# Kernel optimization log

Hardware: AMD Instinct MI355X
Metric: run time of the kernel (lower is better)

Reference implementation:

```python
import jax, jax.numpy as jnp
import numpy as np

ALPHA = 0.2  # LeakyReLU negative slope
NEG_INF = jnp.float32(-9e15)


def gat_layer(h, mask, W, a, concat):
    """Dense GAT layer (pyGAT style). h: [B,N,Fin], mask: [N,N] bool, W: [Fin,Fout], a: [2*Fout,1]."""
    Wh = h @ W                                   # [B,N,Fout]
    F_out = W.shape[-1]
    e_src = Wh @ a[:F_out]                       # [B,N,1]
    e_dst = Wh @ a[F_out:]                       # [B,N,1]
    e = jax.nn.leaky_relu(e_src + jnp.swapaxes(e_dst, -1, -2), ALPHA)  # [B,N,N]
    att = jnp.where(mask, e, NEG_INF)
    att = jax.nn.softmax(att, axis=-1)
    out = att @ Wh                               # [B,N,Fout]
    return jax.nn.elu(out) if concat else out


def setup_inputs() -> dict:
    key = jax.random.key(0)
    ks = jax.random.split(key, 8)
    B, N, nfeat, nhid, nheads, emb, nclass = 4, 2048, 128, 64, 8, 64, 16
    slices = jax.random.normal(ks[0], (B, N, nfeat), jnp.float32)
    adj = jax.random.randint(ks[1], (N, N), 0, 2, jnp.int32)
    s = 1.0 / float(np.sqrt(nfeat))
    Ws = jax.random.uniform(ks[2], (nheads, nfeat, nhid), jnp.float32, -s, s)
    As = jax.random.uniform(ks[3], (nheads, 2 * nhid, 1), jnp.float32, -s, s)
    W1 = jax.random.uniform(ks[4], (nhid * nheads, emb), jnp.float32, -s, s)
    a1 = jax.random.uniform(ks[5], (2 * emb, 1), jnp.float32, -s, s)
    W2 = jax.random.uniform(ks[6], (emb, nclass), jnp.float32, -s, s)
    a2 = jax.random.uniform(ks[7], (2 * nclass, 1), jnp.float32, -s, s)
    return {"slices": slices, "adj": adj, "Ws": Ws, "As": As,
            "W1": W1, "a1": a1, "W2": W2, "a2": a2}


def reference(slices, adj, Ws, As, W1, a1, W2, a2):
    # Eval mode: dropout = 0 (identity).
    mask = adj > 0                               # [N,N], broadcasts over batch
    # Multi-head GAT with concat=True (ELU inside each head), vectorized over heads.
    heads = jax.vmap(lambda W, a: gat_layer(slices, mask, W, a, True))(Ws, As)  # [H,B,N,nhid]
    H, B, N, nh = heads.shape
    x = jnp.moveaxis(heads, 0, 2).reshape(B, N, H * nh)  # concat along features, head-major
    image_feature = jax.nn.elu(gat_layer(x, mask, W1, a1, False))              # [B,N,emb]
    pre = jax.nn.elu(gat_layer(image_feature, mask, W2, a2, False))            # [B,N,nclass]
    pre = pre[:, 0, :]                                                         # [B,nclass]
    return image_feature, pre
```

## Files before the change

### kernel.cpp

```cpp
#include <hip/hip_runtime.h>
#include <hip/hip_bf16.h>
#include <cstdint>


#define NN 2048

typedef float f32x4 __attribute__((ext_vector_type(4)));
typedef __bf16 bf16x8 __attribute__((ext_vector_type(8)));
typedef _Float16 f16;
typedef _Float16 f16x8 __attribute__((ext_vector_type(8)));

__global__ __launch_bounds__(256) void prep_k(
    const int* __restrict__ adj, unsigned char* __restrict__ pm,
    const float* __restrict__ Ws, __bf16* __restrict__ WsFh, __bf16* __restrict__ WsFl,
    const float* __restrict__ W1, __bf16* __restrict__ W1Fh, __bf16* __restrict__ W1Fl,
    unsigned int* __restrict__ ticket) {
  const int bx = blockIdx.x, t = threadIdx.x;
  if (bx == 0 && t == 0) *ticket = 0u;
  if (bx < 2048) {
    const int i = bx;
#pragma unroll
    for (int jt = 0; jt < 8; ++jt) {
      const int j = jt * 256 + t;
      pm[((long)(j >> 5) << 16) + i * 32 + (j & 31)] =
          adj[(long)i * NN + j] > 0 ? 0xFFu : 0u;
    }
  } else if (bx < 2304) {
    const int idx = (bx - 2048) * 256 + t;
    const int inst = idx >> 13;
    const int rem = idx & 8191;
    const int k = rem >> 6, n = rem & 63;
    const float v = Ws[(long)inst * 8192 + rem];
    const __bf16 vh = (__bf16)v;
    const int pos = ((k >> 5) * 4 + (n >> 4)) * 512 + (((k >> 3) & 3) * 16 + (n & 15)) * 8 + (k & 7);
    WsFh[(long)inst * 8192 + pos] = vh;
    WsFl[(long)inst * 8192 + pos] = (__bf16)(v - (float)vh);
  } else {
    const int idx = (bx - 2304) * 256 + t;
    const int k = idx >> 6, n = idx & 63;
    const float v = W1[idx];
    const __bf16 vh = (__bf16)v;
    const int pos = ((k >> 5) * 4 + (n >> 4)) * 512 + (((k >> 3) & 3) * 16 + (n & 15)) * 8 + (k & 7);
    W1Fh[pos] = vh;
    W1Fl[pos] = (__bf16)(v - (float)vh);
  }
}

struct GemmLd {
  float4 a0, a1;
  bf16x8 bh[4], bl[4];
};

__global__ __launch_bounds__(128) void gemm_mfma_k(
    const float* __restrict__ Aall, const __bf16* __restrict__ WFhi,
    const __bf16* __restrict__ WFlo, const float* __restrict__ avecAll,
    f16* __restrict__ WhBAll, float* __restrict__ Eo, float* __restrict__ Go,
    f16* __restrict__ Fo, f16* __restrict__ Ho,
    int K, long aStrideB) {
  const int bid = blockIdx.x;
  const int xcd = bid & 7, r = bid >> 3;
  const int xblk = r & 63, hh = r >> 6;
  const int head = ((xcd >> 2) << 2) + hh;
  const int p = (head << 2) | (xcd & 3);
  const float* A = Aall + (long)(p & 3) * aStrideB;
  const long wfOff = (long)(p >> 2) * K * 64;
  const bf16x8* BhF = (const bf16x8*)(WFhi + wfOff);
  const bf16x8* BlF = (const bf16x8*)(WFlo + wfOff);

  const int t = threadIdx.x, lane = t & 63, wave = t >> 6;
  const int quad = lane >> 4, lm = lane & 15;
  const int i0w = xblk * 32 + wave * 16;
  const float* Arow = A + (long)(i0w + lm) * K;
  const int kBeg = 0, kEnd = K;

  f32x4 acc[4];
#pragma unroll
  for (int nt = 0; nt < 4; ++nt) acc[nt] = (f32x4){0.f, 0.f, 0.f, 0.f};

  auto LOAD = [&](GemmLd& L, int k0) {
    L.a0 = *(const float4*)(Arow + k0 + quad * 8);
    L.a1 = *(const float4*)(Arow + k0 + quad * 8 + 4);
    const int bbase = (k0 >> 5) * 256 + lane;
#pragma unroll
    for (int nt = 0; nt < 4; ++nt) {
      L.bh[nt] = BhF[bbase + nt * 64];
      L.bl[nt] = BlF[bbase + nt * 64];
    }
  };
  auto STEP = [&](const GemmLd& L) {
    const float av8[8] = {L.a0.x, L.a0.y, L.a0.z, L.a0.w, L.a1.x, L.a1.y, L.a1.z, L.a1.w};
    bf16x8 ah, al;
#pragma unroll
    for (int j = 0; j < 8; ++j) {
      const __bf16 h = (__bf16)av8[j];
      ah[j] = h;
      al[j] = (__bf16)(av8[j] - (float)h);
    }
#pragma unroll
    for (int nt = 0; nt < 4; ++nt) {
      acc[nt] = __builtin_amdgcn_mfma_f32_16x16x32_bf16(ah, L.bh[nt], acc[nt], 0, 0, 0);
      acc[nt] = __builtin_amdgcn_mfma_f32_16x16x32_bf16(al, L.bh[nt], acc[nt], 0, 0, 0);
      acc[nt] = __builtin_amdgcn_mfma_f32_16x16x32_bf16(ah, L.bl[nt], acc[nt], 0, 0, 0);
    }
  };

  GemmLd La, Lb;
  LOAD(La, kBeg);
  for (int k0 = kBeg; k0 < kEnd; k0 += 64) {
    LOAD(Lb, k0 + 32);
    STEP(La);
    LOAD(La, (k0 + 64 < kEnd) ? k0 + 64 : kBeg);
    STEP(Lb);
  }

  const float* av = avecAll + (long)(p >> 2) * 128;
  f16* WhB = WhBAll + (long)p * NN * 64;
  float* E = Eo + (long)p * NN;
  float* G = Go + (long)p * NN;
  f16* F = Fo + (long)p * NN;
  f16* Hh = Ho + (long)p * NN;

  float alo[4], ahi[4];
#pragma unroll
  for (int nt = 0; nt < 4; ++nt) {
    alo[nt] = av[nt * 16 + lm];
    ahi[nt] = av[64 + nt * 16 + lm];
  }
#pragma unroll
  for (int reg = 0; reg < 4; ++reg) {
    float es = 0.f, ed = 0.f;
#pragma unroll
    for (int nt = 0; nt < 4; ++nt) {
      es += acc[nt][reg] * alo[nt];
      ed += acc[nt][reg] * ahi[nt];
    }
#pragma unroll
    for (int m = 1; m < 16; m <<= 1) {
      es += __shfl_xor(es, m);
      ed += __shfl_xor(ed, m);
    }
    if (lm == 0) {
      const int r2 = i0w + quad * 4 + reg;
      E[r2] = __expf(es);
      G[r2] = __expf(0.2f * es);
      F[r2] = (f16)__expf(ed);
      Hh[r2] = (f16)__expf(0.2f * ed);
    }
  }

  const int r0 = i0w + quad * 4;
  const long base = ((long)(r0 >> 5) * 4) * 512 + (((r0 >> 3) & 3) * 16 + lm) * 8 + (r0 & 7);
#pragma unroll
  for (int nt = 0; nt < 4; ++nt) {
    union { f16 h[4]; uint2 u; } pk;
#pragma unroll
    for (int q = 0; q < 4; ++q) pk.h[q] = (f16)acc[nt][q];
    *(uint2*)(WhB + base + nt * 512) = pk.u;
  }
}

__global__ __launch_bounds__(512) void gemm2_k(
    const float* __restrict__ Aall, const __bf16* __restrict__ WFhi,
    const __bf16* __restrict__ WFlo, const float* __restrict__ avec,
    f16* __restrict__ WhBAll, float* __restrict__ Eo, float* __restrict__ Go,
    f16* __restrict__ Fo, f16* __restrict__ Ho) {
  const int p = blockIdx.y;
  const float* A = Aall + (long)p * NN * 512;
  const bf16x8* BhF = (const bf16x8*)WFhi;
  const bf16x8* BlF = (const bf16x8*)WFlo;
  const int t = threadIdx.x, lane = t & 63, wave = t >> 6;
  const int ks = wave & 3, rh = wave >> 2;
  const int quad = lane >> 4, lm = lane & 15;
  const int i0 = blockIdx.x * 32;
  const float* Arow = A + (long)(i0 + rh * 16 + lm) * 512;
  const int kBeg = ks * 128, kEnd = kBeg + 128;

  f32x4 acc[4];
#pragma unroll
  for (int nt = 0; nt < 4; ++nt) acc[nt] = (f32x4){0.f, 0.f, 0.f, 0.f};

  auto LOAD = [&](GemmLd& L, int k0) {
    L.a0 = *(const float4*)(Arow + k0 + quad * 8);
    L.a1 = *(const float4*)(Arow + k0 + quad * 8 + 4);
    const int bbase = (k0 >> 5) * 256 + lane;
#pragma unroll
    for (int nt = 0; nt < 4; ++nt) {
      L.bh[nt] = BhF[bbase + nt * 64];
      L.bl[nt] = BlF[bbase + nt * 64];
    }
  };
  auto STEP = [&](const GemmLd& L) {
    const float av8[8] = {L.a0.x, L.a0.y, L.a0.z, L.a0.w, L.a1.x, L.a1.y, L.a1.z, L.a1.w};
    bf16x8 ah, al;
#pragma unroll
    for (int j = 0; j < 8; ++j) {
      const __bf16 h = (__bf16)av8[j];
      ah[j] = h;
      al[j] = (__bf16)(av8[j] - (float)h);
    }
#pragma unroll
    for (int nt = 0; nt < 4; ++nt) {
      acc[nt] = __builtin_amdgcn_mfma_f32_16x16x32_bf16(ah, L.bh[nt], acc[nt], 0, 0, 0);
      acc[nt] = __builtin_amdgcn_mfma_f32_16x16x32_bf16(al, L.bh[nt], acc[nt], 0, 0, 0);
      acc[nt] = __builtin_amdgcn_mfma_f32_16x16x32_bf16(ah, L.bl[nt], acc[nt], 0, 0, 0);
    }
  };

  GemmLd La, Lb;
  LOAD(La, kBeg);
  for (int k0 = kBeg; k0 < kEnd; k0 += 64) {
    LOAD(Lb, k0 + 32);
    STEP(La);
    LOAD(La, (k0 + 64 < kEnd) ? k0 + 64 : kBeg);
    STEP(Lb);
  }

  __shared__ __align__(16) float red[8][4][64][4];
#pragma unroll
  for (int nt = 0; nt < 4; ++nt) *(f32x4*)&red[wave][nt][lane][0] = acc[nt];
  __syncthreads();

  const int n = lane, rgrp = wave;
  const int rh2 = rgrp >> 2, q2 = rgrp & 3;
  const int ln = q2 * 16 + (n & 15), ntq = n >> 4;
  f32x4 c4 = *(const f32x4*)&red[rh2 * 4 + 0][ntq][ln][0];
#pragma unroll
  for (int ksum = 1; ksum < 4; ++ksum)
    c4 += *(const f32x4*)&red[rh2 * 4 + ksum][ntq][ln][0];

  f32x4 es4 = c4 * avec[n];
  f32x4 ed4 = c4 * avec[64 + n];
#pragma unroll
  for (int m = 1; m < 64; m <<= 1) {
#pragma unroll
    for (int q = 0; q < 4; ++q) {
      es4[q] += __shfl_xor(es4[q], m);
      ed4[q] += __shfl_xor(ed4[q], m);
    }
  }
  const int row0 = i0 + rgrp * 4;
  if (n == 0) {
#pragma unroll
    for (int reg = 0; reg < 4; ++reg) {
      const int row = row0 + reg;
      Eo[(long)p * NN + row] = __expf(es4[reg]);
      Go[(long)p * NN + row] = __expf(0.2f * es4[reg]);
      Fo[(long)p * NN + row] = (f16)__expf(ed4[reg]);
      Ho[(long)p * NN + row] = (f16)__expf(0.2f * ed4[reg]);
    }
  }
  f16* WhB = WhBAll + (long)p * NN * 64;
  union { f16 h[4]; uint2 u; } pk;
#pragma unroll
  for (int reg = 0; reg < 4; ++reg) pk.h[reg] = (f16)c4[reg];
  const long pos = ((long)(row0 >> 5) * 4 + ntq) * 512 +
                   ((((row0 >> 3) & 3) * 16 + (n & 15)) * 8) + (row0 & 7);
  *(uint2*)(WhB + pos) = pk.u;
}

struct KbLd {
  f16x8 F8, H8;
  f16x8 b[4];
  uint2 m[4];
};

__global__ __launch_bounds__(512, 2) void attn_k(
    const f16* __restrict__ WhBAll, const float* __restrict__ Eb,
    const float* __restrict__ Gb, const f16* __restrict__ Fb,
    const f16* __restrict__ Hb, const unsigned char* __restrict__ pm,
    float* __restrict__ out1, int rowStride, long strideB,
    int jsCount, float* __restrict__ partAcc, float* __restrict__ partSum) {
  const int bid = blockIdx.x;
  int p, js, rowblk;
  if (jsCount == 1) {
    const int xcd = bid & 7, r = bid >> 3;
    p = xcd * 4 + (r & 3);
    rowblk = r >> 2;
    js = 0;
  } else {
    const int xcd = bid & 7;
    const int idx = ((xcd & 1) << 4) + (bid >> 3);
    p = xcd >> 1;
    js = idx >> 3;
    rowblk = idx & 7;
  }
  const f16* WhB = WhBAll + (long)p * NN * 64;
  const float* E = Eb + (long)p * NN;
  const float* G = Gb + (long)p * NN;
  const f16* Fg = Fb + (long)p * NN;
  const f16* Hg = Hb + (long)p * NN;
  const int t = threadIdx.x, lane = t & 63, wave = t >> 6;
  const int rw = wave & 3, half = wave >> 2;
  const int quad = lane >> 4, lm = lane & 15;
  const int i0 = rowblk * 256;
  const int rbase = rw * 64;
  const int span = 64 / jsCount;
  const int nIter = span / 2;
  const int kbBeg = js * span + half * nIter, kbEnd = kbBeg + nIter;

  __shared__ __align__(16) float cmb[20480];

  f16x8 ev[4], gv[4];
#pragma unroll
  for (int g = 0; g < 4; ++g) {
    const int r = i0 + rbase + g * 16 + lm;
    const f16 e = (f16)E[r], gg = (f16)G[r];
#pragma unroll
    for (int j = 0; j < 8; ++j) { ev[g][j] = e; gv[g][j] = gg; }
  }

  f16x8 ones;
#pragma unroll
  for (int j = 0; j < 8; ++j) ones[j] = (lm == 0) ? (f16)1.0f : (f16)0.0f;

  f32x4 acc[4][4], sum[4];
#pragma unroll
  for (int g = 0; g < 4; ++g) {
    sum[g] = (f32x4){0.f, 0.f, 0.f, 0.f};
#pragma unroll
    for (int nt = 0; nt < 4; ++nt) acc[g][nt] = (f32x4){0.f, 0.f, 0.f, 0.f};
  }

  const unsigned char* mp[4];
#pragma unroll
  for (int g = 0; g < 4; ++g)
    mp[g] = pm + (long)(i0 + rbase + g * 16 + lm) * 32 + quad * 8;

  auto LD = [&](KbLd& L, int kb) {
    L.F8 = *(const f16x8*)(Fg + kb * 32 + quad * 8);
    L.H8 = *(const f16x8*)(Hg + kb * 32 + quad * 8);
#pragma unroll
    for (int nt = 0; nt < 4; ++nt)
      L.b[nt] = *(const f16x8*)(WhB + (long)kb * 2048 + (nt * 64 + lane) * 8);
#pragma unroll
    for (int g = 0; g < 4; ++g)
      L.m[g] = *(const uint2*)(mp[g] + ((long)kb << 16));
  };
  auto CP = [&](const KbLd& L) {
    union { f16x8 v; uint4 u4; } A[4];
#pragma unroll
    for (int g = 0; g < 4; ++g) {
      A[g].v = __builtin_elementwise_max(ev[g] * L.F8, gv[g] * L.H8);
      A[g].u4.x &= __builtin_amdgcn_perm(0u, L.m[g].x, 0x01010000u);
      A[g].u4.y &= __builtin_amdgcn_perm(0u, L.m[g].x, 0x03030202u);
      A[g].u4.z &= __builtin_amdgcn_perm(0u, L.m[g].y, 0x01010000u);
      A[g].u4.w &= __builtin_amdgcn_perm(0u, L.m[g].y, 0x03030202u);
    }
    __builtin_amdgcn_s_setprio(1);
#pragma unroll
    for (int nt = 0; nt < 4; ++nt) {
#pragma unroll
      for (int g = 0; g < 4; ++g)
        acc[g][nt] = __builtin_amdgcn_mfma_f32_16x16x32_f16(A[g].v, L.b[nt], acc[g][nt], 0, 0, 0);
    }
#pragma unroll
    for (int g = 0; g < 4; ++g)
      sum[g] = __builtin_amdgcn_mfma_f32_16x16x32_f16(A[g].v, ones, sum[g], 0, 0, 0);
    __builtin_amdgcn_s_setprio(0);
  };

  KbLd La, Lb2;
  LD(La, kbBeg);
  for (int kb = kbBeg; kb < kbEnd; kb += 2) {
    LD(Lb2, kb + 1);
    CP(La);
    if (kb + 2 < kbEnd) LD(La, kb + 2);
    CP(Lb2);
  }

  if (half == 1) {
#pragma unroll
    for (int g = 0; g < 4; ++g) {
#pragma unroll
      for (int nt = 0; nt < 4; ++nt)
        *(f32x4*)&cmb[((rw * 20 + g * 4 + nt) * 64 + lane) * 4] = acc[g][nt];
      *(f32x4*)&cmb[((rw * 20 + 16 + g) * 64 + lane) * 4] = sum[g];
    }
  }
  __syncthreads();
  if (half == 1) return;
#pragma unroll
  for (int g = 0; g < 4; ++g) {
#pragma unroll
    for (int nt = 0; nt < 4; ++nt)
      acc[g][nt] += *(const f32x4*)&cmb[((rw * 20 + g * 4 + nt) * 64 + lane) * 4];
    sum[g] += *(const f32x4*)&cmb[((rw * 20 + 16 + g) * 64 + lane) * 4];
  }

  if (jsCount == 1) {
#pragma unroll
    for (int g = 0; g < 4; ++g) {
#pragma unroll
      for (int reg = 0; reg < 4; ++reg) {
        const int row = i0 + rbase + g * 16 + quad * 4 + reg;
        const float ls = __shfl(sum[g][reg], quad * 16);
        const float il = ls > 0.f ? 1.f / ls : 0.f;
#pragma unroll
        for (int nt = 0; nt < 4; ++nt) {
          float v = acc[g][nt][reg] * il;
          v = v > 0.f ? v : expm1f(v);
          const long o = (long)(p & 3) * strideB + (long)row * rowStride + (p >> 2) * 64 + nt * 16 + lm;
          out1[o] = v;
        }
      }
    }
  } else {
    float* pAcc = partAcc + ((long)p * jsCount + js) * NN * 64;
    float* pSum = partSum + ((long)p * jsCount + js) * NN;
#pragma unroll
    for (int g = 0; g < 4; ++g) {
#pragma unroll
      for (int reg = 0; reg < 4; ++reg) {
        const int row = i0 + rbase + g * 16 + quad * 4 + reg;
#pragma unroll
        for (int nt = 0; nt < 4; ++nt) pAcc[(long)row * 64 + nt * 16 + lm] = acc[g][nt][reg];
        if (lm == 0) pSum[row] = sum[g][reg];
      }
    }
  }
}

__global__ __launch_bounds__(256) void combine_k(const float* __restrict__ partAcc,
                                                 const float* __restrict__ partSum,
                                                 float* __restrict__ img,
                                                 float* __restrict__ out, int JS) {
  const long idx = (long)blockIdx.x * 256 + threadIdx.x;
  const int cg = idx & 15;
  const int row = (int)((idx >> 4) & (NN - 1));
  const int inst = (int)(idx >> 15);
  f32x4 v = (f32x4){0.f, 0.f, 0.f, 0.f};
  float s = 0.f;
  for (int js = 0; js < JS; ++js) {
    const long b = ((long)inst * JS + js) * NN;
    v += *(const f32x4*)(partAcc + (b + row) * 64 + cg * 4);
    s += partSum[b + row];
  }
  const float il = s > 0.f ? 1.f / s : 0.f;
  f32x4 r;
#pragma unroll
  for (int q = 0; q < 4; ++q) {
    float x = v[q] * il;
    r[q] = x > 0.f ? x : expm1f(x);
  }
  const long o = ((long)inst * NN + row) * 64 + cg * 4;
  *(f32x4*)(img + o) = r;
  *(f32x4*)(out + o) = r;
}

__global__ __launch_bounds__(256) void layer3a_k(
    const float* __restrict__ img, const float* __restrict__ W2,
    const float* __restrict__ a2, const unsigned char* __restrict__ pm,
    float* __restrict__ pOut , float* __restrict__ outPre,
    unsigned int* __restrict__ ticket) {
  const int bb = blockIdx.x, chunk = blockIdx.y, t = threadIdx.x;
  const float* A = img + (long)bb * NN * 64;
  __shared__ float w2alo[64], w2ahi[64];
  __shared__ float W2s[64][17];
  __shared__ float redc[4][17];
  __shared__ int lastS;
  if (t < 64) {
    float sl = 0.f, sh = 0.f;
#pragma unroll
    for (int c = 0; c < 16; ++c) {
      const float wv = W2[t * 16 + c];
      W2s[t][c] = wv;
      sl += wv * a2[c];
      sh += wv * a2[16 + c];
    }
    w2alo[t] = sl;
    w2ahi[t] = sh;
  }
  __syncthreads();

  float es = 0.f;
#pragma unroll 16
  for (int k = 0; k < 64; ++k) es += A[k] * w2alo[k];

  const int j = chunk * 256 + t;
  float arow[64];
#pragma unroll
  for (int q = 0; q < 16; ++q) *(f32x4*)(arow + q * 4) = *(const f32x4*)(A + (long)j * 64 + q * 4);
  float ed = 0.f;
#pragma unroll
  for (int k = 0; k < 64; ++k) ed += arow[k] * w2ahi[k];
  float e = es + ed;
  e = fmaxf(e, 0.2f * e);
  const float pv = pm[((long)(j >> 5) << 16) + (j & 31)] ? __expf(e) : 0.f;

  float acc[16];
#pragma unroll
  for (int c = 0; c < 16; ++c) {
    float wh = 0.f;
#pragma unroll
    for (int k = 0; k < 64; ++k) wh += arow[k] * W2s[k][c];
    acc[c] = pv * wh;
  }
  float lsum = pv;

#pragma unroll
  for (int off = 32; off > 0; off >>= 1) {
    lsum += __shfl_down(lsum, off);
#pragma unroll
    for (int c = 0; c < 16; ++c) acc[c] += __shfl_down(acc[c], off);
  }
  if ((t & 63) == 0) {
    const int wv = t >> 6;
#pragma unroll
    for (int c = 0; c < 16; ++c) redc[wv][c] = acc[c];
    redc[wv][16] = lsum;
  }
  __syncthreads();
  if (t < 17) {
    __hip_atomic_store(&pOut[((long)bb * 8 + chunk) * 17 + t],
                       redc[0][t] + redc[1][t] + redc[2][t] + redc[3][t],
                       __ATOMIC_RELAXED, __HIP_MEMORY_SCOPE_AGENT);
  }
  __syncthreads();
  if (t == 0)
    lastS = (__hip_atomic_fetch_add(ticket, 1u, __ATOMIC_ACQ_REL,
                                    __HIP_MEMORY_SCOPE_AGENT) == 31u);
  __syncthreads();
  if (lastS && t < 64) {
    const int b2 = t >> 4, c2 = t & 15;
    float a = 0.f, l = 0.f;
#pragma unroll
    for (int ch = 0; ch < 8; ++ch) {
      a += __hip_atomic_load(&pOut[((long)b2 * 8 + ch) * 17 + c2],
                             __ATOMIC_RELAXED, __HIP_MEMORY_SCOPE_AGENT);
      l += __hip_atomic_load(&pOut[((long)b2 * 8 + ch) * 17 + 16],
                             __ATOMIC_RELAXED, __HIP_MEMORY_SCOPE_AGENT);
    }
    float v = a / l;
    v = v > 0.f ? v : expm1f(v);
    outPre[b2 * 16 + c2] = v;
  }
}

extern "C" void kernel_launch(void* const* d_in, const int* in_sizes, int n_in,
                              void* d_out, int out_size, void* d_ws, size_t ws_size,
                              hipStream_t stream) {
  (void)in_sizes; (void)n_in; (void)out_size; (void)ws_size;
  constexpr int B = 4, N = NN, JS2 = 4;

  const float* slices = (const float*)d_in[0];
  const int* adj = (const int*)d_in[1];
  const float* Ws = (const float*)d_in[2];
  const float* As = (const float*)d_in[3];
  const float* W1 = (const float*)d_in[4];
  const float* a1 = (const float*)d_in[5];
  const float* W2 = (const float*)d_in[6];
  const float* a2 = (const float*)d_in[7];
  float* out = (float*)d_out;

  char* w = (char*)d_ws;
  size_t off = 0;
  auto alloc = [&](size_t bytes) {
    void* ptr = w + off;
    off += (bytes + 255) & ~(size_t)255;
    return ptr;
  };
  unsigned char* pm = (unsigned char*)alloc((size_t)64 * 65536);
  __bf16* WsFh = (__bf16*)alloc((size_t)8 * 128 * 64 * 2);
  __bf16* WsFl = (__bf16*)alloc((size_t)8 * 128 * 64 * 2);
  __bf16* W1Fh = (__bf16*)alloc((size_t)512 * 64 * 2);
  __bf16* W1Fl = (__bf16*)alloc((size_t)512 * 64 * 2);
  f16* WhB1 = (f16*)alloc((size_t)32 * N * 64 * 2);
  float* E1 = (float*)alloc((size_t)32 * N * 4);
  float* G1 = (float*)alloc((size_t)32 * N * 4);
  f16* F1 = (f16*)alloc((size_t)32 * N * 2);
  f16* H1 = (f16*)alloc((size_t)32 * N * 2);
  float* x = (float*)alloc((size_t)B * N * 512 * 4);
  f16* WhB2 = (f16*)alloc((size_t)B * N * 64 * 2);
  float* E2 = (float*)alloc((size_t)B * N * 4);
  float* G2 = (float*)alloc((size_t)B * N * 4);
  f16* F2 = (f16*)alloc((size_t)B * N * 2);
  f16* H2 = (f16*)alloc((size_t)B * N * 2);
  float* img = (float*)alloc((size_t)B * N * 64 * 4);
  float* pAcc2 = (float*)alloc((size_t)B * JS2 * N * 64 * 4);
  float* pSum2 = (float*)alloc((size_t)B * JS2 * N * 4);
  float* pL3 = (float*)alloc((size_t)B * 8 * 17 * 4);
  unsigned int* ticket = (unsigned int*)alloc(256);

  prep_k<<<dim3(2432), dim3(256), 0, stream>>>(adj, pm, Ws, WsFh, WsFl, W1, W1Fh, W1Fl, ticket);

  gemm_mfma_k<<<dim3(2048), dim3(128), 0, stream>>>(
      slices, WsFh, WsFl, As, WhB1, E1, G1, F1, H1, 128, (long)N * 128);
  attn_k<<<dim3(256), dim3(512), 0, stream>>>(
      WhB1, E1, G1, F1, H1, pm, x, 512, (long)N * 512,
      1, (float*)nullptr, (float*)nullptr);

  gemm2_k<<<dim3(N / 32, 4), dim3(512), 0, stream>>>(
      x, W1Fh, W1Fl, a1, WhB2, E2, G2, F2, H2);
  attn_k<<<dim3(128), dim3(512), 0, stream>>>(
      WhB2, E2, G2, F2, H2, pm, (float*)nullptr, 64, (long)N * 64,
      JS2, pAcc2, pSum2);
  combine_k<<<dim3(B * N * 16 / 256), dim3(256), 0, stream>>>(pAcc2, pSum2, img, out, JS2);

  layer3a_k<<<dim3(B, 8), dim3(256), 0, stream>>>(img, W2, a2, pm, pL3,
                                                  out + (size_t)B * N * 64, ticket);
}
```

Baseline: 162.9 us.

## Fuse prep kernel into first GEMM with in-LDS weight split conversion

Merges the mask/weight preparation kernel into the first-layer GEMM launch. Extra blocks build the adjacency mask and split W1, while each GEMM block converts its head's Ws slice into bf16 hi/lo pairs in shared memory instead of reading a pre-split global copy. This removes one kernel launch and the global round-trip for the Ws split. In exchange, every GEMM block repeats the 8192-element conversion and uses 32KB of LDS, which can lower occupancy.

Result: slower. 168.5 us (+3.4%).

```diff
diff --git a/kernel.cpp b/kernel.cpp
--- a/kernel.cpp
+++ b/kernel.cpp
@@ -10,68 +10,69 @@
 typedef _Float16 f16;
 typedef _Float16 f16x8 __attribute__((ext_vector_type(8)));
 
-__global__ __launch_bounds__(256) void prep_k(
-    const int* __restrict__ adj, unsigned char* __restrict__ pm,
-    const float* __restrict__ Ws, __bf16* __restrict__ WsFh, __bf16* __restrict__ WsFl,
-    const float* __restrict__ W1, __bf16* __restrict__ W1Fh, __bf16* __restrict__ W1Fl,
-    unsigned int* __restrict__ ticket) {
-  const int bx = blockIdx.x, t = threadIdx.x;
-  if (bx == 0 && t == 0) *ticket = 0u;
-  if (bx < 2048) {
-    const int i = bx;
-#pragma unroll
-    for (int jt = 0; jt < 8; ++jt) {
-      const int j = jt * 256 + t;
-      pm[((long)(j >> 5) << 16) + i * 32 + (j & 31)] =
-          adj[(long)i * NN + j] > 0 ? 0xFFu : 0u;
-    }
-  } else if (bx < 2304) {
-    const int idx = (bx - 2048) * 256 + t;
-    const int inst = idx >> 13;
-    const int rem = idx & 8191;
-    const int k = rem >> 6, n = rem & 63;
-    const float v = Ws[(long)inst * 8192 + rem];
-    const __bf16 vh = (__bf16)v;
-    const int pos = ((k >> 5) * 4 + (n >> 4)) * 512 + (((k >> 3) & 3) * 16 + (n & 15)) * 8 + (k & 7);
-    WsFh[(long)inst * 8192 + pos] = vh;
-    WsFl[(long)inst * 8192 + pos] = (__bf16)(v - (float)vh);
-  } else {
-    const int idx = (bx - 2304) * 256 + t;
-    const int k = idx >> 6, n = idx & 63;
-    const float v = W1[idx];
-    const __bf16 vh = (__bf16)v;
-    const int pos = ((k >> 5) * 4 + (n >> 4)) * 512 + (((k >> 3) & 3) * 16 + (n & 15)) * 8 + (k & 7);
-    W1Fh[pos] = vh;
-    W1Fl[pos] = (__bf16)(v - (float)vh);
-  }
-}
-
 struct GemmLd {
   float4 a0, a1;
   bf16x8 bh[4], bl[4];
 };
 
-__global__ __launch_bounds__(128) void gemm_mfma_k(
-    const float* __restrict__ Aall, const __bf16* __restrict__ WFhi,
-    const __bf16* __restrict__ WFlo, const float* __restrict__ avecAll,
+__global__ __launch_bounds__(128) void front_k(
+    const float* __restrict__ Aall, const int* __restrict__ adj,
+    const float* __restrict__ Ws, const float* __restrict__ avecAll,
+    const float* __restrict__ W1,
+    unsigned char* __restrict__ pm, __bf16* __restrict__ W1Fh, __bf16* __restrict__ W1Fl,
     f16* __restrict__ WhBAll, float* __restrict__ Eo, float* __restrict__ Go,
     f16* __restrict__ Fo, f16* __restrict__ Ho,
-    int K, long aStrideB) {
-  const int bid = blockIdx.x;
-  const int xcd = bid & 7, r = bid >> 3;
+    int K, long aStrideB, unsigned int* __restrict__ ticket) {
+  const int bx = blockIdx.x, t = threadIdx.x;
+
+  if (bx >= 2048) {
+    if (bx < 4096) {
+      const int i = bx - 2048;
+#pragma unroll
+      for (int jt = 0; jt < 16; ++jt) {
+        const int j = jt * 128 + t;
+        pm[((long)(j >> 5) << 16) + i * 32 + (j & 31)] =
+            adj[(long)i * NN + j] > 0 ? 0xFFu : 0u;
+      }
+    } else {
+      if (bx == 4096 && t == 0) *ticket = 0u;
+      const int idx = (bx - 4096) * 128 + t;
+      const int k = idx >> 6, n = idx & 63;
+      const float v = W1[idx];
+      const __bf16 vh = (__bf16)v;
+      const int pos = ((k >> 5) * 4 + (n >> 4)) * 512 + (((k >> 3) & 3) * 16 + (n & 15)) * 8 + (k & 7);
+      W1Fh[pos] = vh;
+      W1Fl[pos] = (__bf16)(v - (float)vh);
+    }
+    return;
+  }
+
+  const int xcd = bx & 7, r = bx >> 3;
   const int xblk = r & 63, hh = r >> 6;
   const int head = ((xcd >> 2) << 2) + hh;
   const int p = (head << 2) | (xcd & 3);
   const float* A = Aall + (long)(p & 3) * aStrideB;
-  const long wfOff = (long)(p >> 2) * K * 64;
-  const bf16x8* BhF = (const bf16x8*)(WFhi + wfOff);
-  const bf16x8* BlF = (const bf16x8*)(WFlo + wfOff);
-
-  const int t = threadIdx.x, lane = t & 63, wave = t >> 6;
+
+  __shared__ __align__(16) __bf16 WsLh[8192], WsLl[8192];
+  {
+    const float* Wsrc = Ws + (long)(p >> 2) * 8192;
+#pragma unroll 8
+    for (int u = 0; u < 64; ++u) {
+      const int e = u * 128 + t;
+      const int k = e >> 6, n = e & 63;
+      const float v = Wsrc[e];
+      const __bf16 vh = (__bf16)v;
+      const int pos = ((k >> 5) * 4 + (n >> 4)) * 512 + (((k >> 3) & 3) * 16 + (n & 15)) * 8 + (k & 7);
+      WsLh[pos] = vh;
+      WsLl[pos] = (__bf16)(v - (float)vh);
+    }
+  }
+  __syncthreads();
+
+  const int lane = t & 63, wave = t >> 6;
   const int quad = lane >> 4, lm = lane & 15;
   const int i0w = xblk * 32 + wave * 16;
   const float* Arow = A + (long)(i0w + lm) * K;
-  const int kBeg = 0, kEnd = K;
 
   f32x4 acc[4];
 #pragma unroll
@@ -83,8 +84,8 @@
     const int bbase = (k0 >> 5) * 256 + lane;
 #pragma unroll
     for (int nt = 0; nt < 4; ++nt) {
-      L.bh[nt] = BhF[bbase + nt * 64];
-      L.bl[nt] = BlF[bbase + nt * 64];
+      L.bh[nt] = *(const bf16x8*)(WsLh + (bbase + nt * 64) * 8);
+      L.bl[nt] = *(const bf16x8*)(WsLl + (bbase + nt * 64) * 8);
     }
   };
   auto STEP = [&](const GemmLd& L) {
@@ -105,11 +106,11 @@
   };
 
   GemmLd La, Lb;
-  LOAD(La, kBeg);
-  for (int k0 = kBeg; k0 < kEnd; k0 += 64) {
+  LOAD(La, 0);
+  for (int k0 = 0; k0 < K; k0 += 64) {
     LOAD(Lb, k0 + 32);
     STEP(La);
-    LOAD(La, (k0 + 64 < kEnd) ? k0 + 64 : kBeg);
+    LOAD(La, (k0 + 64 < K) ? k0 + 64 : 0);
     STEP(Lb);
   }
 
@@ -560,8 +561,6 @@
     return ptr;
   };
   unsigned char* pm = (unsigned char*)alloc((size_t)64 * 65536);
-  __bf16* WsFh = (__bf16*)alloc((size_t)8 * 128 * 64 * 2);
-  __bf16* WsFl = (__bf16*)alloc((size_t)8 * 128 * 64 * 2);
   __bf16* W1Fh = (__bf16*)alloc((size_t)512 * 64 * 2);
   __bf16* W1Fl = (__bf16*)alloc((size_t)512 * 64 * 2);
   f16* WhB1 = (f16*)alloc((size_t)32 * N * 64 * 2);
@@ -581,10 +580,9 @@
   float* pL3 = (float*)alloc((size_t)B * 8 * 17 * 4);
   unsigned int* ticket = (unsigned int*)alloc(256);
 
-  prep_k<<<dim3(2432), dim3(256), 0, stream>>>(adj, pm, Ws, WsFh, WsFl, W1, W1Fh, W1Fl, ticket);
-
-  gemm_mfma_k<<<dim3(2048), dim3(128), 0, stream>>>(
-      slices, WsFh, WsFl, As, WhB1, E1, G1, F1, H1, 128, (long)N * 128);
+  front_k<<<dim3(4352), dim3(128), 0, stream>>>(
+      slices, adj, Ws, As, W1, pm, W1Fh, W1Fl,
+      WhB1, E1, G1, F1, H1, 128, (long)N * 128, ticket);
   attn_k<<<dim3(256), dim3(512), 0, stream>>>(
       WhB1, E1, G1, F1, H1, pm, x, 512, (long)N * 512,
       1, (float*)nullptr, (float*)nullptr);
```
